# Optimization experiments

Hardware: AMD Instinct MI355X
Metric: run time of the kernel (lower is better)

Reference implementation:

```python
import jax, jax.numpy as jnp
import numpy as np

B, T, F, H = 4096, 48, 64, 128


def _uniform(key, shape, stdv):
    return jax.random.uniform(key, shape, jnp.float32, -stdv, stdv)


def setup_inputs() -> dict:
    key = jax.random.key(0)
    ks = jax.random.split(key, 24)
    values = jax.random.normal(ks[0], (B, T, F), jnp.float32)
    masks = (jax.random.uniform(ks[1], (B, T, F)) < 0.8).astype(jnp.float32)
    deltas = jax.random.uniform(ks[2], (B, T, F), jnp.float32)
    sH = 1.0 / np.sqrt(H)
    sF = 1.0 / np.sqrt(F)
    inp = {
        "values": values, "masks": masks, "deltas": deltas,
        # TemporalDecay h: W [H, F], b [H] (stdv = 1/sqrt(out=H))
        "Wdh": _uniform(ks[3], (H, F), sH), "bdh": _uniform(ks[4], (H,), sH),
        # TemporalDecay x (diag): W [F, F], b [F]
        "Wdx": _uniform(ks[5], (F, F), sF), "bdx": _uniform(ks[6], (F,), sF),
        # hist_reg: Linear(H -> F)
        "Wh": _uniform(ks[7], (F, H), sH), "bh": _uniform(ks[8], (F,), sH),
        # feat_reg: masked F x F
        "Wf": _uniform(ks[9], (F, F), sF), "bf": _uniform(ks[10], (F,), sF),
        # weight_combine: Linear(2F -> F)
        "Wc": _uniform(ks[11], (F, 2 * F), 1.0 / np.sqrt(2 * F)),
        "bc": _uniform(ks[12], (F,), 1.0 / np.sqrt(2 * F)),
        # LSTMCell(2F -> H): gates in PyTorch order i, f, g, o
        "W_ih": _uniform(ks[13], (4 * H, 2 * F), sH),
        "W_hh": _uniform(ks[14], (4 * H, H), sH),
        "b_ih": _uniform(ks[15], (4 * H,), sH),
        "b_hh": _uniform(ks[16], (4 * H,), sH),
        # out: Linear(H -> 1)
        "Wo": _uniform(ks[17], (1, H), sH), "bo": _uniform(ks[18], (1,), sH),
    }
    return inp


def reference(values, masks, deltas, Wdh, bdh, Wdx, bdx, Wh, bh, Wf, bf,
              Wc, bc, W_ih, W_hh, b_ih, b_hh, Wo, bo):
    impute_weight = 1.0
    b, t, f = values.shape
    h_dim = Wdh.shape[0]
    eye = jnp.eye(f, dtype=values.dtype)
    Wdx_m = Wdx * eye            # diagonal temporal decay
    Wf_m = Wf * (1.0 - eye)

    def step(carry, xt):
        h, c, loss = carry
        x, m, d = xt  # each [B, F]
        gamma_h = jnp.exp(-jax.nn.relu(d @ Wdh.T + bdh))        # [B, H]
        gamma_x = jnp.exp(-jax.nn.relu(d @ Wdx_m.T + bdx))      # [B, F]
        h = h * gamma_h
        x_h = h @ Wh.T + bh
        denom = jnp.sum(m) + 1e-5
        loss = loss + jnp.sum(jnp.abs(x - x_h) * m) / denom
        x_c = m * x + (1.0 - m) * x_h
        z_h = x_c @ Wf_m.T + bf
        loss = loss + jnp.sum(jnp.abs(x - z_h) * m) / denom
        alpha = jnp.concatenate([gamma_x, m], axis=1) @ Wc.T + bc
        c_h = alpha * z_h + (1.0 - alpha) * x_h
        loss = loss + jnp.sum(jnp.abs(x - c_h) * m) / denom
        c_c = m * x + (1.0 - m) * c_h
        inputs = jnp.concatenate([c_c, m], axis=1)  # [B, 2F]
        gates = inputs @ W_ih.T + b_ih + h @ W_hh.T + b_hh
        i_g, f_g, g_g, o_g = jnp.split(gates, 4, axis=1)
        c = jax.nn.sigmoid(f_g) * c + jax.nn.sigmoid(i_g) * jnp.tanh(g_g)
        h = jax.nn.sigmoid(o_g) * jnp.tanh(c)
        return (h, c, loss), c_c

    init = (jnp.zeros((b, h_dim), values.dtype),
            jnp.zeros((b, h_dim), values.dtype),
            jnp.zeros((), values.dtype))
    xs = (jnp.swapaxes(values, 0, 1),
          jnp.swapaxes(masks, 0, 1),
          jnp.swapaxes(deltas, 0, 1))
    (h, c, x_loss), imps = jax.lax.scan(step, init, xs)
    imputations = jnp.swapaxes(imps, 0, 1)  # [B, T, F]
    predictions = h @ Wo.T + bo             # [B, 1]
    return x_loss * impute_weight, imputations, predictions
```

## Files before the change

### kernel.cpp

```cpp
#include <hip/hip_runtime.h>
#include <hip/hip_bf16.h>
#include <math.h>

#define BB 4096
#define TT 48
#define FF 64
#define HH 128
#define ROWS 16
#define NT 512
#define NBLK (BB / ROWS)

typedef __attribute__((ext_vector_type(8))) short short8;
typedef __attribute__((ext_vector_type(4))) float f32x4;

#define MFMA(a, b, c) __builtin_amdgcn_mfma_f32_16x16x32_bf16((a), (b), (c), 0, 0, 0)

__device__ __forceinline__ float sigm(float x) { return 1.f / (1.f + __expf(-x)); }
__device__ __forceinline__ float tanh_f(float x) { return 2.f / (1.f + __expf(-2.f * x)) - 1.f; }

__global__ __launch_bounds__(256) void prep_kernel(
    const float* __restrict__ W_ih, const float* __restrict__ W_hh,
    const float* __restrict__ Wdh,  const float* __restrict__ Wh,
    const float* __restrict__ Wf,   const float* __restrict__ Wc,
    __hip_bfloat16* __restrict__ frags) {
    const int idx = blockIdx.x * 256 + threadIdx.x;
    float v;
    if (idx < 131072) {
        const int jj = idx & 7;
        const int lane = (idx >> 3) & 63;
        const int ks = (idx >> 9) & 7;
        const int tile = idx >> 12;
        const int n = tile * 16 + (lane & 15);
        const int k = ks * 32 + ((lane >> 4) << 3) + jj;
        v = (k < 128) ? W_ih[n * 128 + k] : W_hh[n * 128 + (k - 128)];
    } else {
        const int u = idx - 131072;
        const int jj = u & 7;
        const int lane = (u >> 3) & 63;
        const int lq = lane & 15, q8 = (lane >> 4) << 3;
        if (u < 8192) {
            const int ks = (u >> 9) & 1, nt = u >> 10;
            const int n = nt * 16 + lq, k = ks * 32 + q8 + jj;
            v = Wdh[n * 64 + k];
        } else if (u < 16384) {
            const int uu = u - 8192;
            const int ks = (uu >> 9) & 3, nt = uu >> 11;
            const int n = nt * 16 + lq, k = ks * 32 + q8 + jj;
            v = Wh[n * 128 + k];
        } else if (u < 20480) {
            const int uu = u - 16384;
            const int ks = (uu >> 9) & 1, nt = uu >> 10;
            const int n = nt * 16 + lq, k = ks * 32 + q8 + jj;
            v = (k == n) ? 0.f : Wf[n * 64 + k];
        } else {
            const int uu = u - 20480;
            const int ks = (uu >> 9) & 3, nt = uu >> 11;
            const int n = nt * 16 + lq, k = ks * 32 + q8 + jj;
            v = Wc[n * 128 + k];
        }
    }
    frags[idx] = __float2bfloat16(v);
}

__global__ __launch_bounds__(256) void denom1_kernel(const float* __restrict__ masks,
                                                     float* __restrict__ partials) {
    const int t = blockIdx.x >> 5;
    const int s = blockIdx.x & 31;
    const int tid = threadIdx.x;
    float acc = 0.f;
    #pragma unroll
    for (int k = 0; k < 8; ++k) {
        const int i = k * 256 + tid;
        const int b = s * 128 + (i >> 4);
        const int f = (i & 15) << 2;
        const float4 v = *(const float4*)&masks[((size_t)b * TT + t) * FF + f];
        acc += v.x + v.y + v.z + v.w;
    }
    #pragma unroll
    for (int off = 32; off; off >>= 1) acc += __shfl_down(acc, off, 64);
    __shared__ float red[4];
    if ((tid & 63) == 0) red[tid >> 6] = acc;
    __syncthreads();
    if (tid == 0) partials[blockIdx.x] = red[0] + red[1] + red[2] + red[3];
}

__global__ __launch_bounds__(64) void denom2_kernel(const float* __restrict__ partials,
                                                    float* __restrict__ inv_denom) {
    const int t = threadIdx.x;
    if (t < TT) {
        float s = 0.f;
        #pragma unroll
        for (int i = 0; i < 32; ++i) s += partials[t * 32 + i];
        inv_denom[t] = 1.f / (s + 1e-5f);
    }
}

__global__ __launch_bounds__(NT, 2) void rits_kernel(
    const float* __restrict__ values, const float* __restrict__ masks,
    const float* __restrict__ deltas,
    const float* __restrict__ Wdx, const float* __restrict__ bdx,
    const float* __restrict__ bdh, const float* __restrict__ bh,
    const float* __restrict__ bf,  const float* __restrict__ bc,
    const float* __restrict__ b_ih, const float* __restrict__ b_hh,
    const float* __restrict__ Wo,  const float* __restrict__ bo,
    const __hip_bfloat16* __restrict__ frags,
    const float* __restrict__ inv_denom,
    float* __restrict__ ws_lossblk,
    float* __restrict__ out_imp, float* __restrict__ out_pred)
{
    __shared__ short8 whh_frag[8192];
    __shared__ __hip_bfloat16 dbuf[ROWS][72];
    __shared__ __hip_bfloat16 gxbuf[ROWS][72];
    __shared__ __hip_bfloat16 mbuf[ROWS][72];
    __shared__ __hip_bfloat16 xcbuf[ROWS][72];
    __shared__ __hip_bfloat16 ccbuf[ROWS][72];
    __shared__ __hip_bfloat16 hbufB[ROWS][136];
    __shared__ float x_lds[ROWS][65];
    __shared__ float m_lds[ROWS][65];
    __shared__ float redl[8];

    const int tid = threadIdx.x;
    const int bid = blockIdx.x;
    const int b0 = bid * ROWS;
    const int lane = tid & 63;
    const int wv = tid >> 6;
    const int quad = lane >> 4;
    const int lq = lane & 15;
    const int wv3 = wv & 3;

    const float wdx_l = Wdx[lane * (FF + 1)];
    const float bdx_l = bdx[lane];

    const int j_ln = wv * 16 + lq;
    const float bdh_w = bdh[j_ln];
    const float bI = b_ih[j_ln]       + b_hh[j_ln];
    const float bF = b_ih[128 + j_ln] + b_hh[128 + j_ln];
    const float bG = b_ih[256 + j_ln] + b_hh[256 + j_ln];
    const float bO = b_ih[384 + j_ln] + b_hh[384 + j_ln];

    const int f46 = wv3 * 16 + lq;
    const float bh_f = bh[f46];
    const float bf_f = bf[f46];
    const float bc_f = bc[f46];

    const short8* f8 = (const short8*)frags;

    short8 Bgam[2], Bal[4], Bxh[4], Bzh[2];
    #pragma unroll
    for (int ks = 0; ks < 2; ++ks) Bgam[ks] = f8[16384 + ((wv * 2 + ks) << 6) + lane];
    #pragma unroll
    for (int ks = 0; ks < 4; ++ks) Bal[ks] = f8[18944 + ((wv3 * 4 + ks) << 6) + lane];
    #pragma unroll
    for (int ks = 0; ks < 4; ++ks) Bxh[ks] = f8[17408 + ((wv3 * 4 + ks) << 6) + lane];
    #pragma unroll
    for (int ks = 0; ks < 2; ++ks) Bzh[ks] = f8[18432 + ((wv3 * 2 + ks) << 6) + lane];

    short8 Bcc[4][2], Bm[4][2];
    #pragma unroll
    for (int g = 0; g < 4; ++g) {
        #pragma unroll
        for (int kk = 0; kk < 2; ++kk) {
            Bcc[g][kk] = f8[(((g * 8 + wv) * 8 + kk)     << 6) + lane];
            Bm[g][kk]  = f8[(((g * 8 + wv) * 8 + 2 + kk) << 6) + lane];
        }
    }
    for (int i = tid; i < 8192; i += NT) {
        const int slot = i >> 6, ln = i & 63;
        const int g = slot >> 5, rem = slot & 31, j = rem >> 2, kk = rem & 3;
        whh_frag[i] = f8[(((g * 8 + j) * 8 + 4 + kk) << 6) + ln];
    }
    const int wbase = (wv << 8) + lane;

    float c_reg[4], h_reg[4];
    #pragma unroll
    for (int r = 0; r < 4; ++r) { c_reg[r] = 0.f; h_reg[r] = 0.f; }
    float loss_acc = 0.f;

    const int base0 = ((b0 + wv) * TT) * FF + lane;
    const int base1 = ((b0 + wv + 8) * TT) * FF + lane;
    const int imp0  = ((b0 + quad * 4) * TT) * FF + f46;

    for (int i = tid; i < ROWS * 136; i += NT) ((unsigned short*)hbufB)[i] = 0;
    float xn0 = values[base0], mn0 = masks[base0], dn0 = deltas[base0];
    float xn1 = values[base1], mn1 = masks[base1], dn1 = deltas[base1];
    {
        const int r0 = wv, r1 = wv + 8;
        x_lds[r0][lane] = xn0; m_lds[r0][lane] = mn0;
        gxbuf[r0][lane] = __float2bfloat16(__expf(-fmaxf(fmaf(dn0, wdx_l, bdx_l), 0.f)));
        mbuf[r0][lane]  = __float2bfloat16(mn0);
        x_lds[r1][lane] = xn1; m_lds[r1][lane] = mn1;
        gxbuf[r1][lane] = __float2bfloat16(__expf(-fmaxf(fmaf(dn1, wdx_l, bdx_l), 0.f)));
        mbuf[r1][lane]  = __float2bfloat16(mn1);
    }
    __syncthreads();

    for (int t = 0; t < TT; ++t) {
        const float invd = inv_denom[t];

        {
            const int tn = (t < TT - 1) ? t + 1 : t;
            const int o0 = base0 + tn * FF, o1 = base1 + tn * FF;
            xn0 = values[o0]; mn0 = masks[o0]; dn0 = deltas[o0];
            xn1 = values[o1]; mn1 = masks[o1]; dn1 = deltas[o1];
        }
        f32x4 xacc = {0.f,0.f,0.f,0.f}, aa = {0.f,0.f,0.f,0.f};
        if (wv < 4) {
            #pragma unroll
            for (int ks = 0; ks < 4; ++ks) {
                const short8 a = *(const short8*)&hbufB[lq][ks * 32 + quad * 8];
                xacc = MFMA(a, Bxh[ks], xacc);
            }
            #pragma unroll
            for (int ks = 0; ks < 2; ++ks) {
                const short8 a = *(const short8*)&gxbuf[lq][ks * 32 + quad * 8];
                aa = MFMA(a, Bal[ks], aa);
            }
            #pragma unroll
            for (int ks = 2; ks < 4; ++ks) {
                const short8 a = *(const short8*)&mbuf[lq][(ks - 2) * 32 + quad * 8];
                aa = MFMA(a, Bal[ks], aa);
            }
        }
        f32x4 gacc0 = {0.f,0.f,0.f,0.f}, gacc1 = {0.f,0.f,0.f,0.f};
        f32x4 gacc2 = {0.f,0.f,0.f,0.f}, gacc3 = {0.f,0.f,0.f,0.f};
        #pragma unroll
        for (int kk = 0; kk < 4; ++kk) {
            const short8 a = *(const short8*)&hbufB[lq][kk * 32 + quad * 8];
            gacc0 = MFMA(a, whh_frag[wbase + 0    + kk * 64], gacc0);
            gacc1 = MFMA(a, whh_frag[wbase + 2048 + kk * 64], gacc1);
            gacc2 = MFMA(a, whh_frag[wbase + 4096 + kk * 64], gacc2);
            gacc3 = MFMA(a, whh_frag[wbase + 6144 + kk * 64], gacc3);
        }
        float al_r[4], xv_r[4], mv_r[4], xh_r[4];
        float stepsum = 0.f;
        if (wv < 4) {
            #pragma unroll
            for (int r = 0; r < 4; ++r) {
                al_r[r] = aa[r] + bc_f;
                const int row = quad * 4 + r;
                const float xh = xacc[r] + bh_f;
                xh_r[r] = xh;
                const float xv = x_lds[row][f46], mv = m_lds[row][f46];
                xv_r[r] = xv; mv_r[r] = mv;
                stepsum += mv * fabsf(xv - xh);
                xcbuf[row][f46] = __float2bfloat16(fmaf(mv, xv, (1.f - mv) * xh));
            }
        }
        __syncthreads();

        f32x4 acc5 = {0.f,0.f,0.f,0.f};
        if (wv < 4) {
            #pragma unroll
            for (int ks = 0; ks < 2; ++ks) {
                const short8 a = *(const short8*)&xcbuf[lq][ks * 32 + quad * 8];
                acc5 = MFMA(a, Bzh[ks], acc5);
            }
        }
        #pragma unroll
        for (int kk = 0; kk < 2; ++kk) {
            const short8 a = *(const short8*)&mbuf[lq][kk * 32 + quad * 8];
            gacc0 = MFMA(a, Bm[0][kk], gacc0);
            gacc1 = MFMA(a, Bm[1][kk], gacc1);
            gacc2 = MFMA(a, Bm[2][kk], gacc2);
            gacc3 = MFMA(a, Bm[3][kk], gacc3);
        }
        dbuf[wv][lane]     = __float2bfloat16(dn0);
        dbuf[wv + 8][lane] = __float2bfloat16(dn1);
        if (wv < 4) {
            #pragma unroll
            for (int r = 0; r < 4; ++r) {
                const int row = quad * 4 + r;
                const float zh = acc5[r] + bf_f;
                stepsum += mv_r[r] * fabsf(xv_r[r] - zh);
                const float alpha = al_r[r];
                const float ch = fmaf(alpha, zh, (1.f - alpha) * xh_r[r]);
                stepsum += mv_r[r] * fabsf(xv_r[r] - ch);
                const float cc = fmaf(mv_r[r], xv_r[r], (1.f - mv_r[r]) * ch);
                ccbuf[row][f46] = __float2bfloat16(cc);
                out_imp[imp0 + r * (TT * FF) + t * FF] = cc;
            }
        }
        loss_acc = fmaf(stepsum, invd, loss_acc);
        __syncthreads();

        f32x4 ga = {0.f,0.f,0.f,0.f};
        #pragma unroll
        for (int ks = 0; ks < 2; ++ks) {
            const short8 a = *(const short8*)&dbuf[lq][ks * 32 + quad * 8];
            ga = MFMA(a, Bgam[ks], ga);
        }
        #pragma unroll
        for (int kk = 0; kk < 2; ++kk) {
            const short8 a = *(const short8*)&ccbuf[lq][kk * 32 + quad * 8];
            gacc0 = MFMA(a, Bcc[0][kk], gacc0);
            gacc1 = MFMA(a, Bcc[1][kk], gacc1);
            gacc2 = MFMA(a, Bcc[2][kk], gacc2);
            gacc3 = MFMA(a, Bcc[3][kk], gacc3);
        }
        {
            const int r0 = wv, r1 = wv + 8;
            x_lds[r0][lane] = xn0; m_lds[r0][lane] = mn0;
            gxbuf[r0][lane] = __float2bfloat16(__expf(-fmaxf(fmaf(dn0, wdx_l, bdx_l), 0.f)));
            mbuf[r0][lane]  = __float2bfloat16(mn0);
            x_lds[r1][lane] = xn1; m_lds[r1][lane] = mn1;
            gxbuf[r1][lane] = __float2bfloat16(__expf(-fmaxf(fmaf(dn1, wdx_l, bdx_l), 0.f)));
            mbuf[r1][lane]  = __float2bfloat16(mn1);
        }
        #pragma unroll
        for (int r = 0; r < 4; ++r) {
            const float ig = sigm(gacc0[r] + bI);
            const float fg = sigm(gacc1[r] + bF);
            const float gg = tanh_f(gacc2[r] + bG);
            const float og = sigm(gacc3[r] + bO);
            c_reg[r] = fmaf(fg, c_reg[r], ig * gg);
            h_reg[r] = og * tanh_f(c_reg[r]);
            const float gh = __expf(-fmaxf(ga[r] + bdh_w, 0.f));
            hbufB[quad * 4 + r][j_ln] = __float2bfloat16(h_reg[r] * gh);
        }
        __syncthreads();
    }

    #pragma unroll
    for (int r = 0; r < 4; ++r)
        hbufB[quad * 4 + r][j_ln] = __float2bfloat16(h_reg[r]);
    __syncthreads();
    {
        const int r = tid >> 5, l = tid & 31;
        float s = 0.f;
        #pragma unroll
        for (int k = l; k < HH; k += 32) s += __bfloat162float(hbufB[r][k]) * Wo[k];
        #pragma unroll
        for (int off = 16; off; off >>= 1) s += __shfl_down(s, off, 32);
        if (l == 0) out_pred[b0 + r] = s + bo[0];
    }
    #pragma unroll
    for (int off = 32; off; off >>= 1) loss_acc += __shfl_down(loss_acc, off, 64);
    if (lane == 0) redl[wv] = loss_acc;
    __syncthreads();
    if (tid == 0) {
        float s = 0.f;
        #pragma unroll
        for (int w = 0; w < 8; ++w) s += redl[w];
        ws_lossblk[bid] = s;
    }
}

__global__ __launch_bounds__(256) void final_kernel(const float* __restrict__ ws_lossblk,
                                                    float* __restrict__ out_loss) {
    const int tid = threadIdx.x;
    float s = ws_lossblk[tid];
    #pragma unroll
    for (int off = 32; off; off >>= 1) s += __shfl_down(s, off, 64);
    __shared__ float red[4];
    if ((tid & 63) == 0) red[tid >> 6] = s;
    __syncthreads();
    if (tid == 0) out_loss[0] = red[0] + red[1] + red[2] + red[3];
}

extern "C" void kernel_launch(void* const* d_in, const int* in_sizes, int n_in,
                              void* d_out, int out_size, void* d_ws, size_t ws_size,
                              hipStream_t stream) {
    const float* values = (const float*)d_in[0];
    const float* masks  = (const float*)d_in[1];
    const float* deltas = (const float*)d_in[2];
    const float* Wdh  = (const float*)d_in[3];
    const float* bdh  = (const float*)d_in[4];
    const float* Wdx  = (const float*)d_in[5];
    const float* bdx  = (const float*)d_in[6];
    const float* Wh   = (const float*)d_in[7];
    const float* bh   = (const float*)d_in[8];
    const float* Wf   = (const float*)d_in[9];
    const float* bf   = (const float*)d_in[10];
    const float* Wc   = (const float*)d_in[11];
    const float* bc   = (const float*)d_in[12];
    const float* W_ih = (const float*)d_in[13];
    const float* W_hh = (const float*)d_in[14];
    const float* b_ih = (const float*)d_in[15];
    const float* b_hh = (const float*)d_in[16];
    const float* Wo   = (const float*)d_in[17];
    const float* bo   = (const float*)d_in[18];

    __hip_bfloat16* frags = (__hip_bfloat16*)d_ws;
    float* inv_denom  = (float*)((char*)d_ws + 320 * 1024);
    float* partials   = inv_denom + 64;
    float* ws_lossblk = partials + 2048;

    float* out_loss = (float*)d_out;
    float* out_imp  = out_loss + 1;
    float* out_pred = out_imp + (size_t)BB * TT * FF;

    prep_kernel<<<624, 256, 0, stream>>>(W_ih, W_hh, Wdh, Wh, Wf, Wc, frags);
    denom1_kernel<<<TT * 32, 256, 0, stream>>>(masks, partials);
    denom2_kernel<<<1, 64, 0, stream>>>(partials, inv_denom);
    rits_kernel<<<NBLK, NT, 0, stream>>>(
        values, masks, deltas, Wdx, bdx, bdh, bh, bf, bc,
        b_ih, b_hh, Wo, bo, frags, inv_denom, ws_lossblk, out_imp, out_pred);
    final_kernel<<<1, 256, 0, stream>>>(ws_lossblk, out_loss);
}
```

Baseline: 326.1 us.

## Warp-specialize RITS kernel into LSTM, imputation and alpha wave groups

```diff
diff --git a/kernel.cpp b/kernel.cpp
--- a/kernel.cpp
+++ b/kernel.cpp
@@ -7,7 +7,7 @@
 #define FF 64
 #define HH 128
 #define ROWS 16
-#define NT 512
+#define NT 1024
 #define NBLK (BB / ROWS)
 
 typedef __attribute__((ext_vector_type(8))) short short8;
@@ -95,7 +95,7 @@
     }
 }
 
-__global__ __launch_bounds__(NT, 2) void rits_kernel(
+__global__ __launch_bounds__(NT) void rits_kernel(
     const float* __restrict__ values, const float* __restrict__ masks,
     const float* __restrict__ deltas,
     const float* __restrict__ Wdx, const float* __restrict__ bdx,
@@ -117,7 +117,8 @@
     __shared__ __hip_bfloat16 hbufB[ROWS][136];
     __shared__ float x_lds[ROWS][65];
     __shared__ float m_lds[ROWS][65];
-    __shared__ float redl[8];
+    __shared__ float albuf[ROWS][68];
+    __shared__ float redl[16];
 
     const int tid = threadIdx.x;
     const int bid = blockIdx.x;
@@ -126,205 +127,250 @@
     const int wv = tid >> 6;
     const int quad = lane >> 4;
     const int lq = lane & 15;
-    const int wv3 = wv & 3;
-
-    const float wdx_l = Wdx[lane * (FF + 1)];
-    const float bdx_l = bdx[lane];
-
-    const int j_ln = wv * 16 + lq;
-    const float bdh_w = bdh[j_ln];
-    const float bI = b_ih[j_ln]       + b_hh[j_ln];
-    const float bF = b_ih[128 + j_ln] + b_hh[128 + j_ln];
-    const float bG = b_ih[256 + j_ln] + b_hh[256 + j_ln];
-    const float bO = b_ih[384 + j_ln] + b_hh[384 + j_ln];
-
-    const int f46 = wv3 * 16 + lq;
-    const float bh_f = bh[f46];
-    const float bf_f = bf[f46];
-    const float bc_f = bc[f46];
 
     const short8* f8 = (const short8*)frags;
 
-    short8 Bgam[2], Bal[4], Bxh[4], Bzh[2];
-    #pragma unroll
-    for (int ks = 0; ks < 2; ++ks) Bgam[ks] = f8[16384 + ((wv * 2 + ks) << 6) + lane];
-    #pragma unroll
-    for (int ks = 0; ks < 4; ++ks) Bal[ks] = f8[18944 + ((wv3 * 4 + ks) << 6) + lane];
-    #pragma unroll
-    for (int ks = 0; ks < 4; ++ks) Bxh[ks] = f8[17408 + ((wv3 * 4 + ks) << 6) + lane];
-    #pragma unroll
-    for (int ks = 0; ks < 2; ++ks) Bzh[ks] = f8[18432 + ((wv3 * 2 + ks) << 6) + lane];
-
-    short8 Bcc[4][2], Bm[4][2];
-    #pragma unroll
-    for (int g = 0; g < 4; ++g) {
-        #pragma unroll
-        for (int kk = 0; kk < 2; ++kk) {
-            Bcc[g][kk] = f8[(((g * 8 + wv) * 8 + kk)     << 6) + lane];
-            Bm[g][kk]  = f8[(((g * 8 + wv) * 8 + 2 + kk) << 6) + lane];
-        }
-    }
     for (int i = tid; i < 8192; i += NT) {
         const int slot = i >> 6, ln = i & 63;
         const int g = slot >> 5, rem = slot & 31, j = rem >> 2, kk = rem & 3;
         whh_frag[i] = f8[(((g * 8 + j) * 8 + 4 + kk) << 6) + ln];
     }
-    const int wbase = (wv << 8) + lane;
-
-    float c_reg[4], h_reg[4];
-    #pragma unroll
-    for (int r = 0; r < 4; ++r) { c_reg[r] = 0.f; h_reg[r] = 0.f; }
+    for (int i = tid; i < ROWS * 136; i += NT) ((unsigned short*)hbufB)[i] = 0;
+    __syncthreads();
+
     float loss_acc = 0.f;
 
-    const int base0 = ((b0 + wv) * TT) * FF + lane;
-    const int base1 = ((b0 + wv + 8) * TT) * FF + lane;
-    const int imp0  = ((b0 + quad * 4) * TT) * FF + f46;
-
-    for (int i = tid; i < ROWS * 136; i += NT) ((unsigned short*)hbufB)[i] = 0;
-    float xn0 = values[base0], mn0 = masks[base0], dn0 = deltas[base0];
-    float xn1 = values[base1], mn1 = masks[base1], dn1 = deltas[base1];
-    {
-        const int r0 = wv, r1 = wv + 8;
-        x_lds[r0][lane] = xn0; m_lds[r0][lane] = mn0;
-        gxbuf[r0][lane] = __float2bfloat16(__expf(-fmaxf(fmaf(dn0, wdx_l, bdx_l), 0.f)));
-        mbuf[r0][lane]  = __float2bfloat16(mn0);
-        x_lds[r1][lane] = xn1; m_lds[r1][lane] = mn1;
-        gxbuf[r1][lane] = __float2bfloat16(__expf(-fmaxf(fmaf(dn1, wdx_l, bdx_l), 0.f)));
-        mbuf[r1][lane]  = __float2bfloat16(mn1);
-    }
-    __syncthreads();
-
-    for (int t = 0; t < TT; ++t) {
-        const float invd = inv_denom[t];
-
-        {
-            const int tn = (t < TT - 1) ? t + 1 : t;
-            const int o0 = base0 + tn * FF, o1 = base1 + tn * FF;
-            xn0 = values[o0]; mn0 = masks[o0]; dn0 = deltas[o0];
-            xn1 = values[o1]; mn1 = masks[o1]; dn1 = deltas[o1];
+    if (wv < 8) {
+        const int j_ln = wv * 16 + lq;
+        const float bdh_w = bdh[j_ln];
+        const float bI = b_ih[j_ln]       + b_hh[j_ln];
+        const float bF = b_ih[128 + j_ln] + b_hh[128 + j_ln];
+        const float bG = b_ih[256 + j_ln] + b_hh[256 + j_ln];
+        const float bO = b_ih[384 + j_ln] + b_hh[384 + j_ln];
+        short8 Bgam[2];
+        #pragma unroll
+        for (int ks = 0; ks < 2; ++ks) Bgam[ks] = f8[16384 + ((wv * 2 + ks) << 6) + lane];
+        const int wbase = (wv << 8) + lane;
+        const int gbase = (wv << 9) + lane;
+
+        float c_reg[4], h_reg[4];
+        #pragma unroll
+        for (int r = 0; r < 4; ++r) { c_reg[r] = 0.f; h_reg[r] = 0.f; }
+
+        __syncthreads();
+        for (int t = 0; t < TT; ++t) {
+            short8 Bm[4][2];
+            #pragma unroll
+            for (int g = 0; g < 4; ++g)
+                #pragma unroll
+                for (int kk = 0; kk < 2; ++kk)
+                    Bm[g][kk] = f8[gbase + (g << 12) + ((2 + kk) << 6)];
+            f32x4 gacc0 = {0.f,0.f,0.f,0.f}, gacc1 = {0.f,0.f,0.f,0.f};
+            f32x4 gacc2 = {0.f,0.f,0.f,0.f}, gacc3 = {0.f,0.f,0.f,0.f};
+            #pragma unroll
+            for (int kk = 0; kk < 4; ++kk) {
+                const short8 a = *(const short8*)&hbufB[lq][kk * 32 + quad * 8];
+                gacc0 = MFMA(a, whh_frag[wbase + 0    + kk * 64], gacc0);
+                gacc1 = MFMA(a, whh_frag[wbase + 2048 + kk * 64], gacc1);
+                gacc2 = MFMA(a, whh_frag[wbase + 4096 + kk * 64], gacc2);
+                gacc3 = MFMA(a, whh_frag[wbase + 6144 + kk * 64], gacc3);
+            }
+            __syncthreads();
+
+            short8 Bcc[4][2];
+            #pragma unroll
+            for (int g = 0; g < 4; ++g)
+                #pragma unroll
+                for (int kk = 0; kk < 2; ++kk)
+                    Bcc[g][kk] = f8[gbase + (g << 12) + (kk << 6)];
+            #pragma unroll
+            for (int kk = 0; kk < 2; ++kk) {
+                const short8 a = *(const short8*)&mbuf[lq][kk * 32 + quad * 8];
+                gacc0 = MFMA(a, Bm[0][kk], gacc0);
+                gacc1 = MFMA(a, Bm[1][kk], gacc1);
+                gacc2 = MFMA(a, Bm[2][kk], gacc2);
+                gacc3 = MFMA(a, Bm[3][kk], gacc3);
+            }
+            __syncthreads();
+
+            f32x4 ga = {0.f,0.f,0.f,0.f};
+            #pragma unroll
+            for (int ks = 0; ks < 2; ++ks) {
+                const short8 a = *(const short8*)&dbuf[lq][ks * 32 + quad * 8];
+                ga = MFMA(a, Bgam[ks], ga);
+            }
+            #pragma unroll
+            for (int kk = 0; kk < 2; ++kk) {
+                const short8 a = *(const short8*)&ccbuf[lq][kk * 32 + quad * 8];
+                gacc0 = MFMA(a, Bcc[0][kk], gacc0);
+                gacc1 = MFMA(a, Bcc[1][kk], gacc1);
+                gacc2 = MFMA(a, Bcc[2][kk], gacc2);
+                gacc3 = MFMA(a, Bcc[3][kk], gacc3);
+            }
+            #pragma unroll
+            for (int r = 0; r < 4; ++r) {
+                const float ig = sigm(gacc0[r] + bI);
+                const float fg = sigm(gacc1[r] + bF);
+                const float gg = tanh_f(gacc2[r] + bG);
+                const float og = sigm(gacc3[r] + bO);
+                c_reg[r] = fmaf(fg, c_reg[r], ig * gg);
+                h_reg[r] = og * tanh_f(c_reg[r]);
+                const float gh = __expf(-fmaxf(ga[r] + bdh_w, 0.f));
+                hbufB[quad * 4 + r][j_ln] = __float2bfloat16(h_reg[r] * gh);
+            }
+            __syncthreads();
         }
-        f32x4 xacc = {0.f,0.f,0.f,0.f}, aa = {0.f,0.f,0.f,0.f};
-        if (wv < 4) {
+        #pragma unroll
+        for (int r = 0; r < 4; ++r)
+            hbufB[quad * 4 + r][j_ln] = __float2bfloat16(h_reg[r]);
+
+    } else if (wv < 12) {
+        const int cw = wv - 8;
+        const int f46 = (wv & 3) * 16 + lq;
+        const float bh_f = bh[f46];
+        const float bf_f = bf[f46];
+        short8 Bxh[4], Bzh[2];
+        #pragma unroll
+        for (int ks = 0; ks < 4; ++ks) Bxh[ks] = f8[17408 + (((wv & 3) * 4 + ks) << 6) + lane];
+        #pragma unroll
+        for (int ks = 0; ks < 2; ++ks) Bzh[ks] = f8[18432 + (((wv & 3) * 2 + ks) << 6) + lane];
+        const float wdx_l = Wdx[lane * (FF + 1)];
+        const float bdx_l = bdx[lane];
+        const int base0 = ((b0 + cw) * TT) * FF + lane;
+        const int base1 = ((b0 + cw + 8) * TT) * FF + lane;
+        const int imp0  = ((b0 + quad * 4) * TT) * FF + f46;
+
+        float xn0 = values[base0], mn0 = masks[base0], dn0 = deltas[base0];
+        float xn1 = values[base1], mn1 = masks[base1], dn1 = deltas[base1];
+        x_lds[cw][lane] = xn0; m_lds[cw][lane] = mn0;
+        gxbuf[cw][lane] = __float2bfloat16(__expf(-fmaxf(fmaf(dn0, wdx_l, bdx_l), 0.f)));
+        mbuf[cw][lane]  = __float2bfloat16(mn0);
+        x_lds[cw + 8][lane] = xn1; m_lds[cw + 8][lane] = mn1;
+        gxbuf[cw + 8][lane] = __float2bfloat16(__expf(-fmaxf(fmaf(dn1, wdx_l, bdx_l), 0.f)));
+        mbuf[cw + 8][lane]  = __float2bfloat16(mn1);
+
+        __syncthreads();
+        for (int t = 0; t < TT; ++t) {
+            const float invd = inv_denom[t];
+            {
+                const int tn = (t < TT - 1) ? t + 1 : t;
+                const int o0 = base0 + tn * FF, o1 = base1 + tn * FF;
+                xn0 = values[o0]; mn0 = masks[o0]; dn0 = deltas[o0];
+                xn1 = values[o1]; mn1 = masks[o1]; dn1 = deltas[o1];
+            }
+            f32x4 xacc = {0.f,0.f,0.f,0.f};
             #pragma unroll
             for (int ks = 0; ks < 4; ++ks) {
                 const short8 a = *(const short8*)&hbufB[lq][ks * 32 + quad * 8];
                 xacc = MFMA(a, Bxh[ks], xacc);
             }
-            #pragma unroll
-            for (int ks = 0; ks < 2; ++ks) {
-                const short8 a = *(const short8*)&gxbuf[lq][ks * 32 + quad * 8];
-                aa = MFMA(a, Bal[ks], aa);
-            }
-            #pragma unroll
-            for (int ks = 2; ks < 4; ++ks) {
-                const short8 a = *(const short8*)&mbuf[lq][(ks - 2) * 32 + quad * 8];
-                aa = MFMA(a, Bal[ks], aa);
-            }
-        }
-        f32x4 gacc0 = {0.f,0.f,0.f,0.f}, gacc1 = {0.f,0.f,0.f,0.f};
-        f32x4 gacc2 = {0.f,0.f,0.f,0.f}, gacc3 = {0.f,0.f,0.f,0.f};
-        #pragma unroll
-        for (int kk = 0; kk < 4; ++kk) {
-            const short8 a = *(const short8*)&hbufB[lq][kk * 32 + quad * 8];
-            gacc0 = MFMA(a, whh_frag[wbase + 0    + kk * 64], gacc0);
-            gacc1 = MFMA(a, whh_frag[wbase + 2048 + kk * 64], gacc1);
-            gacc2 = MFMA(a, whh_frag[wbase + 4096 + kk * 64], gacc2);
-            gacc3 = MFMA(a, whh_frag[wbase + 6144 + kk * 64], gacc3);
-        }
-        float al_r[4], xv_r[4], mv_r[4], xh_r[4];
-        float stepsum = 0.f;
-        if (wv < 4) {
+            float xh_r[4];
+            float stepsum = 0.f;
             #pragma unroll
             for (int r = 0; r < 4; ++r) {
-                al_r[r] = aa[r] + bc_f;
                 const int row = quad * 4 + r;
                 const float xh = xacc[r] + bh_f;
                 xh_r[r] = xh;
                 const float xv = x_lds[row][f46], mv = m_lds[row][f46];
-                xv_r[r] = xv; mv_r[r] = mv;
                 stepsum += mv * fabsf(xv - xh);
                 xcbuf[row][f46] = __float2bfloat16(fmaf(mv, xv, (1.f - mv) * xh));
             }
-        }
-        __syncthreads();
-
-        f32x4 acc5 = {0.f,0.f,0.f,0.f};
-        if (wv < 4) {
+            __syncthreads();
+
+            f32x4 acc5 = {0.f,0.f,0.f,0.f};
             #pragma unroll
             for (int ks = 0; ks < 2; ++ks) {
                 const short8 a = *(const short8*)&xcbuf[lq][ks * 32 + quad * 8];
                 acc5 = MFMA(a, Bzh[ks], acc5);
             }
-        }
-        #pragma unroll
-        for (int kk = 0; kk < 2; ++kk) {
-            const short8 a = *(const short8*)&mbuf[lq][kk * 32 + quad * 8];
-            gacc0 = MFMA(a, Bm[0][kk], gacc0);
-            gacc1 = MFMA(a, Bm[1][kk], gacc1);
-            gacc2 = MFMA(a, Bm[2][kk], gacc2);
-            gacc3 = MFMA(a, Bm[3][kk], gacc3);
-        }
-        dbuf[wv][lane]     = __float2bfloat16(dn0);
-        dbuf[wv + 8][lane] = __float2bfloat16(dn1);
-        if (wv < 4) {
+            dbuf[cw][lane]     = __float2bfloat16(dn0);
+            dbuf[cw + 8][lane] = __float2bfloat16(dn1);
             #pragma unroll
             for (int r = 0; r < 4; ++r) {
                 const int row = quad * 4 + r;
                 const float zh = acc5[r] + bf_f;
-                stepsum += mv_r[r] * fabsf(xv_r[r] - zh);
-                const float alpha = al_r[r];
+                const float xv = x_lds[row][f46], mv = m_lds[row][f46];
+                stepsum += mv * fabsf(xv - zh);
+                const float alpha = albuf[row][f46];
                 const float ch = fmaf(alpha, zh, (1.f - alpha) * xh_r[r]);
-                stepsum += mv_r[r] * fabsf(xv_r[r] - ch);
-                const float cc = fmaf(mv_r[r], xv_r[r], (1.f - mv_r[r]) * ch);
+                stepsum += mv * fabsf(xv - ch);
+                const float cc = fmaf(mv, xv, (1.f - mv) * ch);
                 ccbuf[row][f46] = __float2bfloat16(cc);
                 out_imp[imp0 + r * (TT * FF) + t * FF] = cc;
             }
+            loss_acc = fmaf(stepsum, invd, loss_acc);
+            __syncthreads();
+
+            x_lds[cw][lane] = xn0; m_lds[cw][lane] = mn0;
+            gxbuf[cw][lane] = __float2bfloat16(__expf(-fmaxf(fmaf(dn0, wdx_l, bdx_l), 0.f)));
+            mbuf[cw][lane]  = __float2bfloat16(mn0);
+            x_lds[cw + 8][lane] = xn1; m_lds[cw + 8][lane] = mn1;
+            gxbuf[cw + 8][lane] = __float2bfloat16(__expf(-fmaxf(fmaf(dn1, wdx_l, bdx_l), 0.f)));
+            mbuf[cw + 8][lane]  = __float2bfloat16(mn1);
+            __syncthreads();
         }
-        loss_acc = fmaf(stepsum, invd, loss_acc);
+
+    } else {
+        const int cw = wv - 8;
+        const int f46 = (wv & 3) * 16 + lq;
+        const float bc_f = bc[f46];
+        short8 Bal[4];
+        #pragma unroll
+        for (int ks = 0; ks < 4; ++ks) Bal[ks] = f8[18944 + (((wv & 3) * 4 + ks) << 6) + lane];
+        const float wdx_l = Wdx[lane * (FF + 1)];
+        const float bdx_l = bdx[lane];
+        const int base0 = ((b0 + cw) * TT) * FF + lane;
+        const int base1 = ((b0 + cw + 8) * TT) * FF + lane;
+
+        float xn0 = values[base0], mn0 = masks[base0], dn0 = deltas[base0];
+        float xn1 = values[base1], mn1 = masks[base1], dn1 = deltas[base1];
+        x_lds[cw][lane] = xn0; m_lds[cw][lane] = mn0;
+        gxbuf[cw][lane] = __float2bfloat16(__expf(-fmaxf(fmaf(dn0, wdx_l, bdx_l), 0.f)));
+        mbuf[cw][lane]  = __float2bfloat16(mn0);
+        x_lds[cw + 8][lane] = xn1; m_lds[cw + 8][lane] = mn1;
+        gxbuf[cw + 8][lane] = __float2bfloat16(__expf(-fmaxf(fmaf(dn1, wdx_l, bdx_l), 0.f)));
+        mbuf[cw + 8][lane]  = __float2bfloat16(mn1);
+
         __syncthreads();
-
-        f32x4 ga = {0.f,0.f,0.f,0.f};
-        #pragma unroll
-        for (int ks = 0; ks < 2; ++ks) {
-            const short8 a = *(const short8*)&dbuf[lq][ks * 32 + quad * 8];
-            ga = MFMA(a, Bgam[ks], ga);
+        for (int t = 0; t < TT; ++t) {
+            {
+                const int tn = (t < TT - 1) ? t + 1 : t;
+                const int o0 = base0 + tn * FF, o1 = base1 + tn * FF;
+                xn0 = values[o0]; mn0 = masks[o0]; dn0 = deltas[o0];
+                xn1 = values[o1]; mn1 = masks[o1]; dn1 = deltas[o1];
+            }
+            f32x4 aa = {0.f,0.f,0.f,0.f};
+            #pragma unroll
+            for (int ks = 0; ks < 2; ++ks) {
+                const short8 a = *(const short8*)&gxbuf[lq][ks * 32 + quad * 8];
+                aa = MFMA(a, Bal[ks], aa);
+            }
+            #pragma unroll
+            for (int ks = 2; ks < 4; ++ks) {
+                const short8 a = *(const short8*)&mbuf[lq][(ks - 2) * 32 + quad * 8];
+                aa = MFMA(a, Bal[ks], aa);
+            }
+            #pragma unroll
+            for (int r = 0; r < 4; ++r)
+                albuf[quad * 4 + r][f46] = aa[r] + bc_f;
+            __syncthreads();
+
+            dbuf[cw][lane]     = __float2bfloat16(dn0);
+            dbuf[cw + 8][lane] = __float2bfloat16(dn1);
+            __syncthreads();
+
+            x_lds[cw][lane] = xn0; m_lds[cw][lane] = mn0;
+            gxbuf[cw][lane] = __float2bfloat16(__expf(-fmaxf(fmaf(dn0, wdx_l, bdx_l), 0.f)));
+            mbuf[cw][lane]  = __float2bfloat16(mn0);
+            x_lds[cw + 8][lane] = xn1; m_lds[cw + 8][lane] = mn1;
+            gxbuf[cw + 8][lane] = __float2bfloat16(__expf(-fmaxf(fmaf(dn1, wdx_l, bdx_l), 0.f)));
+            mbuf[cw + 8][lane]  = __float2bfloat16(mn1);
+            __syncthreads();
         }
-        #pragma unroll
-        for (int kk = 0; kk < 2; ++kk) {
-            const short8 a = *(const short8*)&ccbuf[lq][kk * 32 + quad * 8];
-            gacc0 = MFMA(a, Bcc[0][kk], gacc0);
-            gacc1 = MFMA(a, Bcc[1][kk], gacc1);
-            gacc2 = MFMA(a, Bcc[2][kk], gacc2);
-            gacc3 = MFMA(a, Bcc[3][kk], gacc3);
-        }
-        {
-            const int r0 = wv, r1 = wv + 8;
-            x_lds[r0][lane] = xn0; m_lds[r0][lane] = mn0;
-            gxbuf[r0][lane] = __float2bfloat16(__expf(-fmaxf(fmaf(dn0, wdx_l, bdx_l), 0.f)));
-            mbuf[r0][lane]  = __float2bfloat16(mn0);
-            x_lds[r1][lane] = xn1; m_lds[r1][lane] = mn1;
-            gxbuf[r1][lane] = __float2bfloat16(__expf(-fmaxf(fmaf(dn1, wdx_l, bdx_l), 0.f)));
-            mbuf[r1][lane]  = __float2bfloat16(mn1);
-        }
-        #pragma unroll
-        for (int r = 0; r < 4; ++r) {
-            const float ig = sigm(gacc0[r] + bI);
-            const float fg = sigm(gacc1[r] + bF);
-            const float gg = tanh_f(gacc2[r] + bG);
-            const float og = sigm(gacc3[r] + bO);
-            c_reg[r] = fmaf(fg, c_reg[r], ig * gg);
-            h_reg[r] = og * tanh_f(c_reg[r]);
-            const float gh = __expf(-fmaxf(ga[r] + bdh_w, 0.f));
-            hbufB[quad * 4 + r][j_ln] = __float2bfloat16(h_reg[r] * gh);
-        }
-        __syncthreads();
-    }
-
-    #pragma unroll
-    for (int r = 0; r < 4; ++r)
-        hbufB[quad * 4 + r][j_ln] = __float2bfloat16(h_reg[r]);
+    }
+
     __syncthreads();
-    {
+    if (tid < 512) {
         const int r = tid >> 5, l = tid & 31;
         float s = 0.f;
         #pragma unroll
@@ -340,7 +386,7 @@
     if (tid == 0) {
         float s = 0.f;
         #pragma unroll
-        for (int w = 0; w < 8; ++w) s += redl[w];
+        for (int w = 0; w < 16; ++w) s += redl[w];
         ws_lossblk[bid] = s;
     }
 }
```

New measurement: 320.6 us. About the same (-1.7%).
